# Performance work log

Hardware: AMD Instinct MI355X
Metric: run time of the kernel (lower is better)

The kernel has to match this reference:

```python
import jax, jax.numpy as jnp
import numpy as np

N_USERS, N_ITEMS = 100000, 100000
N_NODES = N_USERS + N_ITEMS
N_EDGES = 4000000
USER_DIM, ITEM_DIM = 256, 128
COMMON, HIDDEN, OUT = 64, 64, 32


def setup_inputs() -> dict:
    key = jax.random.key(0)
    ks = jax.random.split(key, 12)
    inp = {
        "user_tensor": jax.random.normal(ks[0], (N_USERS, USER_DIM), jnp.float32),
        "item_tensor": jax.random.normal(ks[1], (N_ITEMS, ITEM_DIM), jnp.float32),
        "edge_index": jax.random.randint(ks[2], (2, N_EDGES), 0, N_NODES, jnp.int64),
        "edge_weight": jax.random.uniform(ks[3], (N_EDGES,), jnp.float32),
        # user_proj / item_proj (nn.Linear: y = x @ W + b)
        "Wu": jax.random.normal(ks[4], (USER_DIM, COMMON), jnp.float32) / np.sqrt(USER_DIM),
        "bu": jnp.zeros((COMMON,), jnp.float32),
        "Wi": jax.random.normal(ks[5], (ITEM_DIM, COMMON), jnp.float32) / np.sqrt(ITEM_DIM),
        "bi": jnp.zeros((COMMON,), jnp.float32),
        # GCNConv layers (linear without bias + separate bias)
        "W1": jax.random.normal(ks[6], (COMMON, HIDDEN), jnp.float32) / np.sqrt(COMMON),
        "b1": jnp.zeros((HIDDEN,), jnp.float32),
        "W2": jax.random.normal(ks[7], (HIDDEN, OUT), jnp.float32) / np.sqrt(HIDDEN),
        "b2": jnp.zeros((OUT,), jnp.float32),
    }
    return inp


def gcn_conv(x, W, b, src, dst, ew, num_nodes):
    """PyG GCNConv: add self-loops (weight 1), symmetric deg norm, transform, scatter-add."""
    x = x @ W  # transform first: [N, out]
    loop = jnp.arange(num_nodes, dtype=src.dtype)
    src2 = jnp.concatenate([src, loop])
    dst2 = jnp.concatenate([dst, loop])
    ew2 = jnp.concatenate([ew, jnp.ones((num_nodes,), x.dtype)])
    deg = jax.ops.segment_sum(ew2, dst2, num_segments=num_nodes)
    dinv = jnp.where(deg > 0, jax.lax.rsqrt(deg), 0.0)
    norm = dinv[src2] * ew2 * dinv[dst2]  # [E+N]
    msgs = x[src2] * norm[:, None]  # gather + scale: [E+N, out]
    return jax.ops.segment_sum(msgs, dst2, num_segments=num_nodes) + b


def reference(user_tensor, item_tensor, edge_index, edge_weight,
              Wu, bu, Wi, bi, W1, b1, W2, b2):
    user_emb = user_tensor @ Wu + bu
    item_emb = item_tensor @ Wi + bi
    x = jnp.concatenate([user_emb, item_emb], axis=0)  # [N_NODES, COMMON]
    src, dst = edge_index[0], edge_index[1]
    x = gcn_conv(x, W1, b1, src, dst, edge_weight, N_NODES)
    x = jax.nn.relu(x)
    x = gcn_conv(x, W2, b2, src, dst, edge_weight, N_NODES)
    return x
```

## Files before the change

### kernel.cpp

```cpp
#include <hip/hip_runtime.h>
#include <hip/hip_bf16.h>

#define N_USERS_C 100000
#define N_ITEMS_C 100000
#define N_NODES_C 200000
#define USER_DIM_C 256
#define ITEM_DIM_C 128
#define COMMON_C 64
#define HIDDEN_C 64
#define OUT_DIM_C 32

#define CB_BITS 8
#define CB_NODES 256
#define NCB ((N_NODES_C + CB_NODES - 1) / CB_NODES)
#define CB_CAP 5632
#define B_THREADS 256
#define B_UNROLL (CB_CAP / B_THREADS)

#define BIN_GRID 512
#define BIN_CHUNK_MAX 8192
#define MAX_EPT 8

#define UBLK 1563

typedef unsigned int uint32;
typedef __bf16 bf16x8 __attribute__((ext_vector_type(8)));
typedef float f32x4 __attribute__((ext_vector_type(4)));



__device__ __forceinline__ float bf2f(ushort u) { return __uint_as_float(((unsigned)u) << 16); }
__device__ __forceinline__ ushort f2bf(float f) {
    unsigned u = __float_as_uint(f);
    return (ushort)((u + 0x7FFFu + ((u >> 16) & 1u)) >> 16);
}
__device__ __forceinline__ void store4(float* p, float a, float b, float c, float d) {
    *(float4*)p = make_float4(a, b, c, d);
}

union ABFrag {
    uint4 q;
    ushort u[8];
    bf16x8 v;
};


__device__ __forceinline__ void wt_one(const float* W, ushort* WT, int K, int N, int i) {
    int k = i / N, n = i % N;
    WT[(size_t)n * K + k] = f2bf(W[i]);
}


__global__ __launch_bounds__(1024) void bin_kernel(
        const int* __restrict__ src, const int* __restrict__ dst,
        const float* __restrict__ ew, int* __restrict__ bucket_cnt,
        uint2* __restrict__ rec2, int E, int chunk,
        const float* __restrict__ Wu, const float* __restrict__ Wi,
        const float* __restrict__ W1, const float* __restrict__ W2,
        ushort* __restrict__ wtU, ushort* __restrict__ wtI,
        ushort* __restrict__ wt1, ushort* __restrict__ wt2) {
    {
        const int SU = USER_DIM_C * 64, SI = ITEM_DIM_C * 64, S1 = 64 * 64, S2 = 64 * 32;
        int i = blockIdx.x * 1024 + threadIdx.x;
        if (i < SU + SI + S1 + S2) {
            if (i < SU) wt_one(Wu, wtU, USER_DIM_C, 64, i);
            else if ((i -= SU) < SI) wt_one(Wi, wtI, ITEM_DIM_C, 64, i);
            else if ((i -= SI) < S1) wt_one(W1, wt1, 64, 64, i);
            else wt_one(W2, wt2, 64, 32, i - S1);
        }
    }

    __shared__ int hist[NCB];
    __shared__ int cur[NCB];
    for (int i = threadIdx.x; i < NCB; i += 1024) hist[i] = 0;
    __syncthreads();
    const int beg = blockIdx.x * chunk;
    const int end = min(E, beg + chunk);

    int dc[MAX_EPT];
#pragma unroll
    for (int s = 0; s < MAX_EPT / 4; ++s) {
        const int e0 = beg + (threadIdx.x << 2) + (s << 12);
        int4 d4 = make_int4(-1, -1, -1, -1);
        if (e0 + 3 < end) {
            d4 = *(const int4*)(dst + e0);
        } else if (e0 < end) {
            d4.x = dst[e0];
            if (e0 + 1 < end) d4.y = dst[e0 + 1];
            if (e0 + 2 < end) d4.z = dst[e0 + 2];
        }
        dc[s * 4 + 0] = d4.x; dc[s * 4 + 1] = d4.y;
        dc[s * 4 + 2] = d4.z; dc[s * 4 + 3] = d4.w;
        if (d4.x >= 0) atomicAdd(&hist[d4.x >> CB_BITS], 1);
        if (d4.y >= 0) atomicAdd(&hist[d4.y >> CB_BITS], 1);
        if (d4.z >= 0) atomicAdd(&hist[d4.z >> CB_BITS], 1);
        if (d4.w >= 0) atomicAdd(&hist[d4.w >> CB_BITS], 1);
    }
    __syncthreads();

    for (int i = threadIdx.x; i < NCB; i += 1024) {
        const int h = hist[i];
        cur[i] = h ? atomicAdd(&bucket_cnt[i], h) : 0;
    }
    __syncthreads();

#pragma unroll
    for (int s = 0; s < MAX_EPT / 4; ++s) {
        const int e0 = beg + (threadIdx.x << 2) + (s << 12);
        if (e0 >= end) continue;
        int4 s4;
        float4 w4;
        if (e0 + 3 < end) {
            s4 = *(const int4*)(src + e0);
            w4 = *(const float4*)(ew + e0);
        } else {
            s4 = make_int4(0, 0, 0, 0);
            w4 = make_float4(0, 0, 0, 0);
            s4.x = src[e0]; w4.x = ew[e0];
            if (e0 + 1 < end) { s4.y = src[e0 + 1]; w4.y = ew[e0 + 1]; }
            if (e0 + 2 < end) { s4.z = src[e0 + 2]; w4.z = ew[e0 + 2]; }
        }
        const int dv[4] = {dc[s * 4 + 0], dc[s * 4 + 1], dc[s * 4 + 2], dc[s * 4 + 3]};
        const int sv[4] = {s4.x, s4.y, s4.z, s4.w};
        const float wv[4] = {w4.x, w4.y, w4.z, w4.w};
#pragma unroll
        for (int k = 0; k < 4; ++k) {
            const int d = dv[k];
            if (d < 0) continue;
            uint32 q = (uint32)(wv[k] * 255.0f + 0.5f);
            if (q > 255u) q = 255u;
            const int b = d >> CB_BITS;
            const int slot = atomicAdd(&cur[b], 1);
            if (slot < CB_CAP)
                rec2[(size_t)b * CB_CAP + slot] =
                    make_uint2((((uint32)sv[k]) << 8) | q, (uint32)d);
        }
    }
}


__global__ __launch_bounds__(B_THREADS) void region_build_kernel(
        const uint2* __restrict__ rec2, const int* __restrict__ bucket_cnt,
        uint32* __restrict__ csr32, int* __restrict__ row_beg,
        int* __restrict__ row_cnt, float* __restrict__ dinv) {
    __shared__ int pk[CB_NODES];
    __shared__ int s[CB_NODES];
    __shared__ int cur[CB_NODES];
    const int cb = blockIdx.x;
    const int node0 = cb << CB_BITS;
    int total = bucket_cnt[cb];
    if (total > CB_CAP) total = CB_CAP;
    const uint2* r = rec2 + (size_t)cb * CB_CAP;

    pk[threadIdx.x] = 0;
    __syncthreads();

    uint2 rr[B_UNROLL];
#pragma unroll
    for (int u = 0; u < B_UNROLL; ++u) {
        const int j = threadIdx.x + u * B_THREADS;
        if (j < total) {
            rr[u] = r[j];
            atomicAdd(&pk[rr[u].y & (CB_NODES - 1)],
                      (int)((1u << 20) | (rr[u].x & 255u)));
        } else {
            rr[u] = make_uint2(0u, 0xFFFFFFFFu);
        }
    }
    __syncthreads();

    const int v = pk[threadIdx.x] >> 20;
    s[threadIdx.x] = v;
    __syncthreads();
#pragma unroll
    for (int off = 1; off < CB_NODES; off <<= 1) {
        const int t = (threadIdx.x >= off) ? s[threadIdx.x - off] : 0;
        __syncthreads();
        s[threadIdx.x] += t;
        __syncthreads();
    }
    {
        const int ex = s[threadIdx.x] - v;
        const int node = node0 + threadIdx.x;
        const int abs0 = cb * (2 * CB_CAP) + ex;
        if (node < N_NODES_C) {
            row_beg[node] = abs0;
            row_cnt[node] = v;
            dinv[node] = rsqrtf(1.0f + (float)(pk[threadIdx.x] & 0xFFFFF) * (1.0f / 255.0f));
        }
        cur[threadIdx.x] = abs0;
    }
    __syncthreads();

#pragma unroll
    for (int u = 0; u < B_UNROLL; ++u) {
        if (rr[u].y != 0xFFFFFFFFu) {
            const int slot = atomicAdd(&cur[rr[u].y & (CB_NODES - 1)], 1);
            csr32[slot] = rr[u].x;
        }
    }
}


template <int K>
__device__ __forceinline__ void fused_proj_body(
        const float* __restrict__ X, const ushort* __restrict__ WT,
        const ushort* __restrict__ wt1, const float* __restrict__ bias,
        const float* __restrict__ dinv, ushort* __restrict__ y1, int node0, int mb,
        ushort (*elds)[72]) {
    constexpr int NK = K / 32;
    const int lane = threadIdx.x & 63;
    const int wave = threadIdx.x >> 6;
    const int lr = lane & 15;
    const int quad = lane >> 4;

    const int M = N_USERS_C;
    const int m0 = mb * 64 + wave * 16;

    int arow = m0 + lr;
    if (arow >= M) arow = M - 1;
    const float* Xr = X + (size_t)arow * K + quad * 8;

    float4 xf[2 * NK];
#pragma unroll
    for (int t = 0; t < NK; ++t) {
        xf[2 * t] = *(const float4*)(Xr + t * 32);
        xf[2 * t + 1] = *(const float4*)(Xr + t * 32 + 4);
    }
    ABFrag xa[NK];
#pragma unroll
    for (int t = 0; t < NK; ++t) {
        xa[t].u[0] = f2bf(xf[2 * t].x); xa[t].u[1] = f2bf(xf[2 * t].y);
        xa[t].u[2] = f2bf(xf[2 * t].z); xa[t].u[3] = f2bf(xf[2 * t].w);
        xa[t].u[4] = f2bf(xf[2 * t + 1].x); xa[t].u[5] = f2bf(xf[2 * t + 1].y);
        xa[t].u[6] = f2bf(xf[2 * t + 1].z); xa[t].u[7] = f2bf(xf[2 * t + 1].w);
    }

    f32x4 acc[4];
#pragma unroll
    for (int nt = 0; nt < 4; ++nt) acc[nt] = (f32x4){0.0f, 0.0f, 0.0f, 0.0f};

#pragma unroll
    for (int t = 0; t < NK; ++t) {
        const int k0 = t * 32 + quad * 8;
#pragma unroll
        for (int nt = 0; nt < 4; ++nt) {
            ABFrag bf;
            bf.q = *(const uint4*)(WT + (size_t)(nt * 16 + lr) * K + k0);
            acc[nt] = __builtin_amdgcn_mfma_f32_16x16x32_bf16(xa[t].v, bf.v, acc[nt], 0, 0, 0);
        }
    }

#pragma unroll
    for (int r = 0; r < 4; ++r) {
        const int row_l = wave * 16 + quad * 4 + r;
#pragma unroll
        for (int nt = 0; nt < 4; ++nt) {
            const int n = nt * 16 + lr;
            elds[row_l][n] = f2bf(acc[nt][r] + bias[n]);
        }
    }
    __syncthreads();

    f32x4 acc2[4];
#pragma unroll
    for (int nt = 0; nt < 4; ++nt) acc2[nt] = (f32x4){0.0f, 0.0f, 0.0f, 0.0f};

#pragma unroll
    for (int kc = 0; kc < 64; kc += 32) {
        const int k0 = kc + quad * 8;
        ABFrag a;
        a.q = *(const uint4*)(&elds[wave * 16 + lr][k0]);
#pragma unroll
        for (int nt = 0; nt < 4; ++nt) {
            ABFrag bf;
            bf.q = *(const uint4*)(wt1 + (size_t)(nt * 16 + lr) * 64 + k0);
            acc2[nt] = __builtin_amdgcn_mfma_f32_16x16x32_bf16(a.v, bf.v, acc2[nt], 0, 0, 0);
        }
    }

#pragma unroll
    for (int r = 0; r < 4; ++r) {
        const int m = m0 + quad * 4 + r;
        if (m < M) {
            const int node = node0 + m;
            const float sc = dinv[node];
#pragma unroll
            for (int nt = 0; nt < 4; ++nt) {
                y1[(size_t)node * 64 + nt * 16 + lr] = f2bf(acc2[nt][r] * sc);
            }
        }
    }
}

__global__ __launch_bounds__(256) void fused_proj_kernel(
        const float* __restrict__ user, const float* __restrict__ item,
        const ushort* __restrict__ wtU, const ushort* __restrict__ wtI,
        const ushort* __restrict__ wt1, const float* __restrict__ bu,
        const float* __restrict__ bi, const float* __restrict__ dinv,
        ushort* __restrict__ y1) {
    __shared__ ushort elds[64][72];
    if (blockIdx.x < UBLK)
        fused_proj_body<USER_DIM_C>(user, wtU, wt1, bu, dinv, y1, 0, blockIdx.x, elds);
    else
        fused_proj_body<ITEM_DIM_C>(item, wtI, wt1, bi, dinv, y1, N_USERS_C,
                                    blockIdx.x - UBLK, elds);
}


__global__ __launch_bounds__(256) void gather_mm_kernel(
        const int* __restrict__ row_beg, const int* __restrict__ row_cnt,
        const uint32* __restrict__ csr, const ushort* __restrict__ y,
        const float* __restrict__ dinv, const float* __restrict__ b,
        const ushort* __restrict__ wt2, ushort* __restrict__ y2) {
    __shared__ ushort hlds[16][72];
    const int g = threadIdx.x >> 4;
    const int c0 = (threadIdx.x & 15) * 4;
    const int node = blockIdx.x * 16 + g;

    const int beg = row_beg[node];
    const int end = beg + row_cnt[node];

    float a0[4] = {0, 0, 0, 0}, a1[4] = {0, 0, 0, 0}, a2[4] = {0, 0, 0, 0}, a3[4] = {0, 0, 0, 0};
    int j = beg;
    for (; j + 4 <= end; j += 4) {
        uint32 e0 = csr[j], e1 = csr[j + 1], e2 = csr[j + 2], e3 = csr[j + 3];
        int s0 = e0 >> 8, s1 = e1 >> 8, s2 = e2 >> 8, s3 = e3 >> 8;
        float c0v = (float)(e0 & 255u) * (1.0f / 255.0f);
        float c1v = (float)(e1 & 255u) * (1.0f / 255.0f);
        float c2v = (float)(e2 & 255u) * (1.0f / 255.0f);
        float c3v = (float)(e3 & 255u) * (1.0f / 255.0f);
        ushort4 u0 = *(const ushort4*)(y + (size_t)s0 * 64 + c0);
        ushort4 u1 = *(const ushort4*)(y + (size_t)s1 * 64 + c0);
        ushort4 u2 = *(const ushort4*)(y + (size_t)s2 * 64 + c0);
        ushort4 u3 = *(const ushort4*)(y + (size_t)s3 * 64 + c0);
        a0[0] += bf2f(u0.x) * c0v; a0[1] += bf2f(u0.y) * c0v;
        a0[2] += bf2f(u0.z) * c0v; a0[3] += bf2f(u0.w) * c0v;
        a1[0] += bf2f(u1.x) * c1v; a1[1] += bf2f(u1.y) * c1v;
        a1[2] += bf2f(u1.z) * c1v; a1[3] += bf2f(u1.w) * c1v;
        a2[0] += bf2f(u2.x) * c2v; a2[1] += bf2f(u2.y) * c2v;
        a2[2] += bf2f(u2.z) * c2v; a2[3] += bf2f(u2.w) * c2v;
        a3[0] += bf2f(u3.x) * c3v; a3[1] += bf2f(u3.y) * c3v;
        a3[2] += bf2f(u3.z) * c3v; a3[3] += bf2f(u3.w) * c3v;
    }
    for (; j < end; ++j) {
        uint32 e = csr[j];
        int s = e >> 8;
        float cv = (float)(e & 255u) * (1.0f / 255.0f);
        ushort4 u = *(const ushort4*)(y + (size_t)s * 64 + c0);
        a0[0] += bf2f(u.x) * cv; a0[1] += bf2f(u.y) * cv;
        a0[2] += bf2f(u.z) * cv; a0[3] += bf2f(u.w) * cv;
    }
    const float di = dinv[node];
    ushort4 us = *(const ushort4*)(y + (size_t)node * 64 + c0);
    float4 bc = *(const float4*)(b + c0);
    float r0 = (((a0[0] + a1[0]) + (a2[0] + a3[0])) + bf2f(us.x)) * di + bc.x;
    float r1 = (((a0[1] + a1[1]) + (a2[1] + a3[1])) + bf2f(us.y)) * di + bc.y;
    float r2 = (((a0[2] + a1[2]) + (a2[2] + a3[2])) + bf2f(us.z)) * di + bc.z;
    float r3 = (((a0[3] + a1[3]) + (a2[3] + a3[3])) + bf2f(us.w)) * di + bc.w;
    r0 = fmaxf(r0, 0.0f); r1 = fmaxf(r1, 0.0f);
    r2 = fmaxf(r2, 0.0f); r3 = fmaxf(r3, 0.0f);

    ushort4 hu;
    hu.x = f2bf(r0); hu.y = f2bf(r1); hu.z = f2bf(r2); hu.w = f2bf(r3);
    *(ushort4*)&hlds[g][c0] = hu;
    __syncthreads();

    if (threadIdx.x < 64) {
        const int lr = threadIdx.x & 15;
        const int quad = threadIdx.x >> 4;
        f32x4 acc[2];
        acc[0] = (f32x4){0.0f, 0.0f, 0.0f, 0.0f};
        acc[1] = (f32x4){0.0f, 0.0f, 0.0f, 0.0f};
#pragma unroll
        for (int kc = 0; kc < 64; kc += 32) {
            const int k0 = kc + quad * 8;
            ABFrag a;
            a.q = *(const uint4*)(&hlds[lr][k0]);
#pragma unroll
            for (int nt = 0; nt < 2; ++nt) {
                ABFrag bf;
                bf.q = *(const uint4*)(wt2 + (size_t)(nt * 16 + lr) * 64 + k0);
                acc[nt] = __builtin_amdgcn_mfma_f32_16x16x32_bf16(a.v, bf.v, acc[nt], 0, 0, 0);
            }
        }
#pragma unroll
        for (int r = 0; r < 4; ++r) {
            const int nd = blockIdx.x * 16 + quad * 4 + r;
            const float sc = dinv[nd];
#pragma unroll
            for (int nt = 0; nt < 2; ++nt) {
                y2[(size_t)nd * 32 + nt * 16 + lr] = f2bf(acc[nt][r] * sc);
            }
        }
    }
}


template <int N, bool RELU, typename TY>
__global__ void gather_kernel(const int* __restrict__ row_beg, const int* __restrict__ row_cnt,
                              const uint32* __restrict__ csr, const ushort* __restrict__ y,
                              const float* __restrict__ dinv, const float* __restrict__ b,
                              TY* __restrict__ out) {
    constexpr int LPN = N / 4;
    const int node = blockIdx.x * (256 / LPN) + threadIdx.x / LPN;
    const int c0 = (threadIdx.x % LPN) * 4;

    const int beg = row_beg[node];
    const int end = beg + row_cnt[node];

    float a0[4] = {0, 0, 0, 0}, a1[4] = {0, 0, 0, 0}, a2[4] = {0, 0, 0, 0}, a3[4] = {0, 0, 0, 0};
    int j = beg;
    for (; j + 4 <= end; j += 4) {
        uint32 e0 = csr[j], e1 = csr[j + 1], e2 = csr[j + 2], e3 = csr[j + 3];
        int s0 = e0 >> 8, s1 = e1 >> 8, s2 = e2 >> 8, s3 = e3 >> 8;
        float c0v = (float)(e0 & 255u) * (1.0f / 255.0f);
        float c1v = (float)(e1 & 255u) * (1.0f / 255.0f);
        float c2v = (float)(e2 & 255u) * (1.0f / 255.0f);
        float c3v = (float)(e3 & 255u) * (1.0f / 255.0f);
        ushort4 u0 = *(const ushort4*)(y + (size_t)s0 * N + c0);
        ushort4 u1 = *(const ushort4*)(y + (size_t)s1 * N + c0);
        ushort4 u2 = *(const ushort4*)(y + (size_t)s2 * N + c0);
        ushort4 u3 = *(const ushort4*)(y + (size_t)s3 * N + c0);
        a0[0] += bf2f(u0.x) * c0v; a0[1] += bf2f(u0.y) * c0v;
        a0[2] += bf2f(u0.z) * c0v; a0[3] += bf2f(u0.w) * c0v;
        a1[0] += bf2f(u1.x) * c1v; a1[1] += bf2f(u1.y) * c1v;
        a1[2] += bf2f(u1.z) * c1v; a1[3] += bf2f(u1.w) * c1v;
        a2[0] += bf2f(u2.x) * c2v; a2[1] += bf2f(u2.y) * c2v;
        a2[2] += bf2f(u2.z) * c2v; a2[3] += bf2f(u2.w) * c2v;
        a3[0] += bf2f(u3.x) * c3v; a3[1] += bf2f(u3.y) * c3v;
        a3[2] += bf2f(u3.z) * c3v; a3[3] += bf2f(u3.w) * c3v;
    }
    for (; j < end; ++j) {
        uint32 e = csr[j];
        int s = e >> 8;
        float cv = (float)(e & 255u) * (1.0f / 255.0f);
        ushort4 u = *(const ushort4*)(y + (size_t)s * N + c0);
        a0[0] += bf2f(u.x) * cv; a0[1] += bf2f(u.y) * cv;
        a0[2] += bf2f(u.z) * cv; a0[3] += bf2f(u.w) * cv;
    }
    const float di = dinv[node];
    ushort4 us = *(const ushort4*)(y + (size_t)node * N + c0);
    float4 bc = *(const float4*)(b + c0);
    float r0 = (((a0[0] + a1[0]) + (a2[0] + a3[0])) + bf2f(us.x)) * di + bc.x;
    float r1 = (((a0[1] + a1[1]) + (a2[1] + a3[1])) + bf2f(us.y)) * di + bc.y;
    float r2 = (((a0[2] + a1[2]) + (a2[2] + a3[2])) + bf2f(us.z)) * di + bc.z;
    float r3 = (((a0[3] + a1[3]) + (a2[3] + a3[3])) + bf2f(us.w)) * di + bc.w;
    if (RELU) {
        r0 = fmaxf(r0, 0.0f); r1 = fmaxf(r1, 0.0f);
        r2 = fmaxf(r2, 0.0f); r3 = fmaxf(r3, 0.0f);
    }
    store4(&out[(size_t)node * N + c0], r0, r1, r2, r3);
}


extern "C" void kernel_launch(void* const* d_in, const int* in_sizes, int n_in,
                              void* d_out, int out_size, void* d_ws, size_t ws_size,
                              hipStream_t stream) {
    const float* user = (const float*)d_in[0];
    const float* item = (const float*)d_in[1];
    const int* ei = (const int*)d_in[2];
    const float* ew = (const float*)d_in[3];
    const float* Wu = (const float*)d_in[4];
    const float* bu = (const float*)d_in[5];
    const float* Wi = (const float*)d_in[6];
    const float* bi = (const float*)d_in[7];
    const float* W1 = (const float*)d_in[8];
    const float* b1 = (const float*)d_in[9];
    const float* W2 = (const float*)d_in[10];
    const float* b2 = (const float*)d_in[11];
    float* out = (float*)d_out;

    const int E = in_sizes[3];
    const int* src = ei;
    const int* dst = ei + E;
    const int NB = N_NODES_C;
    const int nblk = (E > BIN_GRID * BIN_CHUNK_MAX) ? ((E + BIN_CHUNK_MAX - 1) / BIN_CHUNK_MAX)
                                                    : BIN_GRID;
    const int chunk = (((E + nblk - 1) / nblk) + 3) & ~3;

    char* p = (char*)d_ws;
    uint2* rec2 = (uint2*)p;   p += (size_t)NCB * CB_CAP * 8;
    ushort* y1 = (ushort*)p;   p += (size_t)NB * 64 * 2;
    ushort* y2 = (ushort*)p;   p += (size_t)NB * 32 * 2;
    int* bucket_cnt = (int*)p; p += (size_t)NCB * 4;
    int* row_beg = (int*)p;    p += (size_t)NB * 4;
    int* row_cnt = (int*)p;    p += (size_t)NB * 4;
    float* dinv = (float*)p;   p += (size_t)NB * 4;
    ushort* wtU = (ushort*)p;  p += (size_t)USER_DIM_C * 64 * 2;
    ushort* wtI = (ushort*)p;  p += (size_t)ITEM_DIM_C * 64 * 2;
    ushort* wt1 = (ushort*)p;  p += (size_t)64 * 64 * 2;
    ushort* wt2 = (ushort*)p;  p += (size_t)64 * 32 * 2;

    uint32* csr = (uint32*)rec2;

    hipMemsetAsync(bucket_cnt, 0, (size_t)NCB * 4, stream);
    bin_kernel<<<nblk, 1024, 0, stream>>>(src, dst, ew, bucket_cnt, rec2, E, chunk,
                                          Wu, Wi, W1, W2, wtU, wtI, wt1, wt2);
    region_build_kernel<<<NCB, B_THREADS, 0, stream>>>(rec2, bucket_cnt, csr, row_beg, row_cnt,
                                                       dinv);

    fused_proj_kernel<<<2 * UBLK, 256, 0, stream>>>(user, item, wtU, wtI, wt1, bu, bi, dinv, y1);

    gather_mm_kernel<<<NB / 16, 256, 0, stream>>>(row_beg, row_cnt, csr, y1, dinv, b1, wt2, y2);

    gather_kernel<32, false><<<NB / 32, 256, 0, stream>>>(row_beg, row_cnt, csr, y2, dinv, b2, out);
}
```

Before: 486.9 us.

## Stage projection input rows through LDS via global_load_lds and split launches

The projection kernel now copies 64-row by 128-column fp32 tiles of the input into shared memory with direct global-to-LDS loads, so each row is read contiguously. Each wave then reads its MFMA A-fragments from LDS. Before this, each lane made strided per-row float4 global loads. The combined user/item kernel is split into two templated launches, one per input. This adds a larger shared-memory footprint, extra barriers per K phase and one more kernel launch, and removes the in-kernel branch between the two inputs.

```diff
diff --git a/kernel.cpp b/kernel.cpp
--- a/kernel.cpp
+++ b/kernel.cpp
@@ -36,6 +36,12 @@
 }
 __device__ __forceinline__ void store4(float* p, float a, float b, float c, float d) {
     *(float4*)p = make_float4(a, b, c, d);
+}
+
+__device__ __forceinline__ void gload16(const void* g, void* l) {
+    __builtin_amdgcn_global_load_lds(
+        (const __attribute__((address_space(1))) void*)g,
+        (__attribute__((address_space(3))) void*)l, 16, 0, 0);
 }
 
 union ABFrag {
@@ -203,52 +209,57 @@
 
 
 template <int K>
-__device__ __forceinline__ void fused_proj_body(
+__global__ __launch_bounds__(256) void fused_proj_kernel(
         const float* __restrict__ X, const ushort* __restrict__ WT,
         const ushort* __restrict__ wt1, const float* __restrict__ bias,
-        const float* __restrict__ dinv, ushort* __restrict__ y1, int node0, int mb,
-        ushort (*elds)[72]) {
-    constexpr int NK = K / 32;
+        const float* __restrict__ dinv, ushort* __restrict__ y1, int node0) {
+    constexpr int KT = 128;
+    constexpr int RS = KT + 4;
+    constexpr int NPH = K / KT;
+    __shared__ float xlds[64 * RS];
+    __shared__ ushort elds[64][72];
+
     const int lane = threadIdx.x & 63;
     const int wave = threadIdx.x >> 6;
     const int lr = lane & 15;
     const int quad = lane >> 4;
-
     const int M = N_USERS_C;
-    const int m0 = mb * 64 + wave * 16;
-
-    int arow = m0 + lr;
-    if (arow >= M) arow = M - 1;
-    const float* Xr = X + (size_t)arow * K + quad * 8;
-
-    float4 xf[2 * NK];
-#pragma unroll
-    for (int t = 0; t < NK; ++t) {
-        xf[2 * t] = *(const float4*)(Xr + t * 32);
-        xf[2 * t + 1] = *(const float4*)(Xr + t * 32 + 4);
-    }
-    ABFrag xa[NK];
-#pragma unroll
-    for (int t = 0; t < NK; ++t) {
-        xa[t].u[0] = f2bf(xf[2 * t].x); xa[t].u[1] = f2bf(xf[2 * t].y);
-        xa[t].u[2] = f2bf(xf[2 * t].z); xa[t].u[3] = f2bf(xf[2 * t].w);
-        xa[t].u[4] = f2bf(xf[2 * t + 1].x); xa[t].u[5] = f2bf(xf[2 * t + 1].y);
-        xa[t].u[6] = f2bf(xf[2 * t + 1].z); xa[t].u[7] = f2bf(xf[2 * t + 1].w);
-    }
+    const int m0 = blockIdx.x * 64 + wave * 16;
 
     f32x4 acc[4];
 #pragma unroll
     for (int nt = 0; nt < 4; ++nt) acc[nt] = (f32x4){0.0f, 0.0f, 0.0f, 0.0f};
 
-#pragma unroll
-    for (int t = 0; t < NK; ++t) {
-        const int k0 = t * 32 + quad * 8;
-#pragma unroll
-        for (int nt = 0; nt < 4; ++nt) {
-            ABFrag bf;
-            bf.q = *(const uint4*)(WT + (size_t)(nt * 16 + lr) * K + k0);
-            acc[nt] = __builtin_amdgcn_mfma_f32_16x16x32_bf16(xa[t].v, bf.v, acc[nt], 0, 0, 0);
-        }
+    for (int ph = 0; ph < NPH; ++ph) {
+#pragma unroll
+        for (int j = 0; j < 16; ++j) {
+            const int r = wave * 16 + j;
+            int grow = blockIdx.x * 64 + r;
+            if (grow >= M) grow = M - 1;
+            if (lane < 32) {
+                const float* g = X + (size_t)grow * K + ph * KT + lane * 4;
+                gload16(g, xlds + r * RS);
+            }
+        }
+        __syncthreads();
+
+        const float* xr = xlds + (wave * 16 + lr) * RS + quad * 8;
+#pragma unroll
+        for (int t = 0; t < 4; ++t) {
+            const float4 x0 = *(const float4*)(xr + t * 32);
+            const float4 x1 = *(const float4*)(xr + t * 32 + 4);
+            ABFrag a;
+            a.u[0] = f2bf(x0.x); a.u[1] = f2bf(x0.y); a.u[2] = f2bf(x0.z); a.u[3] = f2bf(x0.w);
+            a.u[4] = f2bf(x1.x); a.u[5] = f2bf(x1.y); a.u[6] = f2bf(x1.z); a.u[7] = f2bf(x1.w);
+            const int k0 = ph * KT + t * 32 + quad * 8;
+#pragma unroll
+            for (int nt = 0; nt < 4; ++nt) {
+                ABFrag bf;
+                bf.q = *(const uint4*)(WT + (size_t)(nt * 16 + lr) * K + k0);
+                acc[nt] = __builtin_amdgcn_mfma_f32_16x16x32_bf16(a.v, bf.v, acc[nt], 0, 0, 0);
+            }
+        }
+        __syncthreads();
     }
 
 #pragma unroll
@@ -291,20 +302,6 @@
             }
         }
     }
-}
-
-__global__ __launch_bounds__(256) void fused_proj_kernel(
-        const float* __restrict__ user, const float* __restrict__ item,
-        const ushort* __restrict__ wtU, const ushort* __restrict__ wtI,
-        const ushort* __restrict__ wt1, const float* __restrict__ bu,
-        const float* __restrict__ bi, const float* __restrict__ dinv,
-        ushort* __restrict__ y1) {
-    __shared__ ushort elds[64][72];
-    if (blockIdx.x < UBLK)
-        fused_proj_body<USER_DIM_C>(user, wtU, wt1, bu, dinv, y1, 0, blockIdx.x, elds);
-    else
-        fused_proj_body<ITEM_DIM_C>(item, wtI, wt1, bi, dinv, y1, N_USERS_C,
-                                    blockIdx.x - UBLK, elds);
 }
 
 
@@ -500,7 +497,9 @@
     region_build_kernel<<<NCB, B_THREADS, 0, stream>>>(rec2, bucket_cnt, csr, row_beg, row_cnt,
                                                        dinv);
 
-    fused_proj_kernel<<<2 * UBLK, 256, 0, stream>>>(user, item, wtU, wtI, wt1, bu, bi, dinv, y1);
+    fused_proj_kernel<USER_DIM_C><<<UBLK, 256, 0, stream>>>(user, wtU, wt1, bu, dinv, y1, 0);
+    fused_proj_kernel<ITEM_DIM_C><<<UBLK, 256, 0, stream>>>(item, wtI, wt1, bi, dinv, y1,
+                                                            N_USERS_C);
 
     gather_mm_kernel<<<NB / 16, 256, 0, stream>>>(row_beg, row_cnt, csr, y1, dinv, b1, wt2, y2);
 
```

Measured after the change: 500.7 us. 2.8% more time.
